# Kernel tuning notes

Hardware: AMD Instinct MI355X
Metric: run time of the kernel (lower is better)

The kernel has to match this reference:

```python
import jax, jax.numpy as jnp
import numpy as np


def setup_inputs() -> dict:
    key = jax.random.key(0)
    ks = jax.random.split(key, 6)
    B, T, D, H = 2, 2048, 1024, 16
    dk = D // H
    s = 0.02
    return {
        "x": jax.random.normal(ks[0], (B, T, D), dtype=jnp.float32),
        "Wq": jax.random.normal(ks[1], (H, dk, dk), dtype=jnp.float32) * s,
        "Wk": jax.random.normal(ks[2], (H, dk, dk), dtype=jnp.float32) * s,
        "Wv": jax.random.normal(ks[3], (H, dk, dk), dtype=jnp.float32) * s,
        "Wp": jax.random.normal(ks[4], (D, D), dtype=jnp.float32) * s,
        "bp": jnp.zeros((D,), dtype=jnp.float32),
    }


def reference(x, Wq, Wk, Wv, Wp, bp):
    B, T, D = x.shape
    H, dk, _ = Wq.shape
    # split into heads: [B, H, T, dk]
    xh = x.reshape(B, T, H, dk).transpose(0, 2, 1, 3)
    # per-head torch Linear (y = x @ W^T), all heads at once
    q = jnp.einsum('bhtd,hkd->bhtk', xh, Wq)
    k = jnp.einsum('bhtd,hkd->bhtk', xh, Wk)
    v = jnp.einsum('bhtd,hkd->bhtk', xh, Wv)
    scale = 1.0 / jnp.sqrt(jnp.float32(dk))  # original divides by sqrt(C) with C == d_k
    scores = jnp.einsum('bhqd,bhkd->bhqk', q, k) * scale
    causal = jnp.tril(jnp.ones((T, T), dtype=bool))
    scores = jnp.where(causal[None, None], scores, -jnp.inf)
    attn = jax.nn.softmax(scores, axis=-1)
    out = jnp.einsum('bhqk,bhkd->bhqd', attn, v)  # [B,H,T,dk]
    out = out.transpose(0, 2, 1, 3).reshape(B, T, D)  # concat heads
    return out @ Wp.T + bp
```

## Files before the change

kernel.cpp:

```cpp
#include <hip/hip_runtime.h>
#include <math.h>

#define B_ 2
#define T_ 2048
#define D_ 1024
#define H_ 16
#define DK 64
#define BH_ (B_*H_)

typedef __attribute__((ext_vector_type(8))) short short8;
typedef __attribute__((ext_vector_type(4))) float fragC;

#define MFMA32(A,B,C) __builtin_amdgcn_mfma_f32_16x16x32_bf16((A),(B),(C),0,0,0)

#if defined(__HIP_DEVICE_COMPILE__) && __has_builtin(__builtin_amdgcn_exp2f)
#define EXP2 __builtin_amdgcn_exp2f
#else
#define EXP2 exp2f
#endif

__device__ __forceinline__ unsigned short f2bf(float x) {
    union { float f; unsigned u; } c; c.f = x;
    unsigned r = c.u + 0x7fff + ((c.u >> 16) & 1);
    return (unsigned short)(r >> 16);
}

__device__ __forceinline__ unsigned pack2bf(float a, float b) {
    return (unsigned)f2bf(a) | ((unsigned)f2bf(b) << 16);
}

__device__ __forceinline__ unsigned permpack(float a, float b) {
    union { float f; unsigned u; } ca, cb; ca.f = a; cb.f = b;
    return __builtin_amdgcn_perm(cb.u, ca.u, 0x07060302);
}

__device__ __forceinline__ float truncbf(float x) {
    union { float f; unsigned u; } c; c.f = x;
    c.u &= 0xffff0000u;
    return c.f;
}

__device__ __forceinline__ short8 packbf8(float4 a, float4 b) {
    union { short8 v; unsigned u[4]; } r;
    r.u[0] = pack2bf(a.x, a.y); r.u[1] = pack2bf(a.z, a.w);
    r.u[2] = pack2bf(b.x, b.y); r.u[3] = pack2bf(b.z, b.w);
    return r.v;
}

__device__ __forceinline__ void gload_lds16(const void* g, void* l) {
    __builtin_amdgcn_global_load_lds(
        (const __attribute__((address_space(1))) unsigned int*)g,
        (__attribute__((address_space(3))) unsigned int*)l, 16, 0, 0);
}

__global__ __launch_bounds__(256) void qkv_kernel(
    const float* __restrict__ x,
    const float* __restrict__ Wq, const float* __restrict__ Wk,
    const float* __restrict__ Wv, const float* __restrict__ Wp,
    unsigned short* __restrict__ Wb,
    unsigned short* __restrict__ q, unsigned short* __restrict__ k,
    unsigned short* __restrict__ vt)
{
    __shared__ unsigned short Wl[3*64*64];

    const int bh = blockIdx.x;
    const int b  = bh >> 4, h = bh & 15;
    const int t0 = blockIdx.y * 128;
    const int tid = threadIdx.x;
    const int wave = tid >> 6, lane = tid & 63;
    const int n = lane & 15, quad = lane >> 4;

    {
        const int L = bh + (blockIdx.y << 5);
        const float* src = Wp + (size_t)L*2048 + tid*8;
        float4 a = *(const float4*)src;
        float4 b2 = *(const float4*)(src + 4);
        *(uint4*)(Wb + (size_t)L*2048 + tid*8) =
            make_uint4(pack2bf(a.x, a.y), pack2bf(a.z, a.w),
                       pack2bf(b2.x, b2.y), pack2bf(b2.z, b2.w));
    }

    #pragma unroll
    for (int mat = 0; mat < 3; ++mat) {
        const float* ws = ((mat == 0) ? Wq : (mat == 1) ? Wk : Wv)
                          + (size_t)h * 4096;
        #pragma unroll
        for (int j = 0; j < 2; ++j) {
            const int e = (j*256 + tid) * 8;
            float4 a = *(const float4*)&ws[e];
            float4 b2 = *(const float4*)&ws[e + 4];
            *(uint4*)&Wl[mat*4096 + e] =
                make_uint4(pack2bf(a.x, a.y), pack2bf(a.z, a.w),
                           pack2bf(b2.x, b2.y), pack2bf(b2.z, b2.w));
        }
    }

    const int tw = t0 + wave*32;
    short8 xf[2][2];
    #pragma unroll
    for (int rt = 0; rt < 2; ++rt) {
        const float* xr = &x[((size_t)b*T_ + tw + rt*16 + n)*D_ + h*DK];
        float4 a0 = *(const float4*)&xr[quad*8];
        float4 a1 = *(const float4*)&xr[quad*8 + 4];
        xf[rt][0] = packbf8(a0, a1);
        float4 b0 = *(const float4*)&xr[32 + quad*8];
        float4 b1 = *(const float4*)&xr[32 + quad*8 + 4];
        xf[rt][1] = packbf8(b0, b1);
    }
    __syncthreads();

    const float qsc = 0.125f * 1.44269504088896340736f;
    const int tb0 = blockIdx.y*8 + wave*2;
    #pragma unroll
    for (int mat = 0; mat < 3; ++mat) {
        const int wbase = mat * 4096;
        #pragma unroll
        for (int ct = 0; ct < 4; ++ct) {
            short8 wf0 = *(const short8*)&Wl[wbase + (ct*16 + n)*64 + quad*8];
            short8 wf1 = *(const short8*)&Wl[wbase + (ct*16 + n)*64 + 32 + quad*8];
            if (mat < 2) {
                #pragma unroll
                for (int rt = 0; rt < 2; ++rt) {
                    fragC z = {0.f,0.f,0.f,0.f};
                    z = MFMA32(wf0, xf[rt][0], z);
                    z = MFMA32(wf1, xf[rt][1], z);
                    if (mat == 0) {
                        z[0] *= qsc; z[1] *= qsc; z[2] *= qsc; z[3] *= qsc;
                    }
                    unsigned short* dstg = (mat == 0) ? q : k;
                    unsigned short* dp = &dstg[((size_t)bh*128 + tb0 + rt)*1024
                                               + (ct*2 + (quad>>1))*128 + n*8 + (quad&1)*4];
                    *(uint2*)dp = make_uint2(pack2bf(z[0], z[1]), pack2bf(z[2], z[3]));
                }
            } else {
                uint4 pv4;
                {
                    fragC z = {0.f,0.f,0.f,0.f};
                    z = MFMA32(xf[0][0], wf0, z);
                    z = MFMA32(xf[0][1], wf1, z);
                    pv4.x = pack2bf(z[0], z[1]); pv4.y = pack2bf(z[2], z[3]);
                }
                {
                    fragC z = {0.f,0.f,0.f,0.f};
                    z = MFMA32(xf[1][0], wf0, z);
                    z = MFMA32(xf[1][1], wf1, z);
                    pv4.z = pack2bf(z[0], z[1]); pv4.w = pack2bf(z[2], z[3]);
                }
                const int ktv = tw >> 6, pv = (tw >> 5) & 1;
                unsigned short* dp = &vt[(size_t)bh*131072 + ktv*4096
                                         + ct*1024 + pv*512 + lane*8];
                *(uint4*)dp = pv4;
            }
        }
    }
}

__global__ __launch_bounds__(256, 2) void attn_kernel(
    const unsigned short* __restrict__ q, const unsigned short* __restrict__ k,
    const unsigned short* __restrict__ vt, unsigned short* __restrict__ aout)
{
    __shared__ fragC Os[4][4][4][64];
    __shared__ float Ls[4][4][16];

    const int id = blockIdx.x;
    const int xc = id & 7, p = id >> 3;
    const int jj = p & 3, s = p >> 2, g = s & 7, r = s >> 3;
    const int bh = xc*4 + jj;
    const int qt = (r == 0) ? 31 - g : (r == 1) ? g : (r == 2) ? 23 - g : 8 + g;

    const int b   = bh >> 4, h = bh & 15;
    const int tid = threadIdx.x;
    const int w = tid >> 6, lane = tid & 63;
    const int n = lane & 15, quad = lane >> 4;

    short8 qf[4][2];
    #pragma unroll
    for (int qc = 0; qc < 4; ++qc) {
        const unsigned short* qb = &q[((size_t)bh*128 + qt*4 + qc)*1024 + n*8];
        qf[qc][0] = *(const short8*)&qb[quad*128];
        qf[qc][1] = *(const short8*)&qb[(4 + quad)*128];
    }

    fragC o[4][4];
    #pragma unroll
    for (int qc = 0; qc < 4; ++qc)
        #pragma unroll
        for (int dt = 0; dt < 4; ++dt) o[qc][dt] = (fragC){0.f,0.f,0.f,0.f};
    float lsc[4] = {0.f, 0.f, 0.f, 0.f};

    const unsigned short* kg = &k[(size_t)bh*131072 + lane*8];
    const unsigned short* vg = &vt[(size_t)bh*131072 + lane*8];
    const int nt = qt + 1;

    short8 kf[4][2];
    short8 vv[4][2];

    int t = w;
    if (t < nt) {
        #pragma unroll
        for (int ct = 0; ct < 4; ++ct) {
            kf[ct][0] = *(const short8*)&kg[t*4096 + ct*1024];
            kf[ct][1] = *(const short8*)&kg[t*4096 + ct*1024 + 512];
        }
        #pragma unroll
        for (int dt = 0; dt < 4; ++dt) {
            vv[dt][0] = *(const short8*)&vg[t*4096 + dt*1024];
            vv[dt][1] = *(const short8*)&vg[t*4096 + dt*1024 + 512];
        }
    }

    for (; t < nt; t += 4) {
        const bool diag = (t == qt);
        #pragma unroll
        for (int qc = 0; qc < 4; ++qc) {
            fragC c[4];
            __builtin_amdgcn_s_setprio(1);
            #pragma unroll
            for (int ct = 0; ct < 4; ++ct) {
                fragC z = {0.f,0.f,0.f,0.f};
                z = MFMA32(kf[ct][0], qf[qc][0], z);
                z = MFMA32(kf[ct][1], qf[qc][1], z);
                c[ct] = z;
            }
            __builtin_amdgcn_s_setprio(0);

            if (qc == 3 && t + 4 < nt) {
                #pragma unroll
                for (int ct = 0; ct < 4; ++ct) {
                    kf[ct][0] = *(const short8*)&kg[(t+4)*4096 + ct*1024];
                    kf[ct][1] = *(const short8*)&kg[(t+4)*4096 + ct*1024 + 512];
                }
            }

            union { unsigned u[4]; short8 v; } pb[2];
            float ls = 0.f;
            #pragma unroll
            for (int ct = 0; ct < 4; ++ct) {
                float p0 = EXP2(c[ct][0]), p1 = EXP2(c[ct][1]);
                float p2 = EXP2(c[ct][2]), p3 = EXP2(c[ct][3]);
                if (diag) {
                    const int lim = (qc*16 + n) - (ct*16 + quad*4);
                    if (0 > lim) p0 = 0.f;
                    if (1 > lim) p1 = 0.f;
                    if (2 > lim) p2 = 0.f;
                    if (3 > lim) p3 = 0.f;
                }
                p0 = truncbf(p0); p1 = truncbf(p1);
                p2 = truncbf(p2); p3 = truncbf(p3);
                ls += (p0 + p1) + (p2 + p3);
                pb[ct >> 1].u[(ct & 1)*2]     = permpack(p0, p1);
                pb[ct >> 1].u[(ct & 1)*2 + 1] = permpack(p2, p3);
            }
            lsc[qc] += ls;

            __builtin_amdgcn_s_setprio(1);
            #pragma unroll
            for (int pv = 0; pv < 2; ++pv) {
                #pragma unroll
                for (int dt = 0; dt < 4; ++dt)
                    o[qc][dt] = MFMA32(vv[dt][pv], pb[pv].v, o[qc][dt]);
            }
            __builtin_amdgcn_s_setprio(0);
        }

        if (t + 4 < nt) {
            #pragma unroll
            for (int dt = 0; dt < 4; ++dt) {
                vv[dt][0] = *(const short8*)&vg[(t+4)*4096 + dt*1024];
                vv[dt][1] = *(const short8*)&vg[(t+4)*4096 + dt*1024 + 512];
            }
        }
    }

    #pragma unroll
    for (int qc = 0; qc < 4; ++qc) {
        lsc[qc] += __shfl_xor(lsc[qc], 16);
        lsc[qc] += __shfl_xor(lsc[qc], 32);
    }

    #pragma unroll
    for (int qc = 0; qc < 4; ++qc) {
        #pragma unroll
        for (int dt = 0; dt < 4; ++dt)
            Os[w][qc][dt][lane] = o[qc][dt];
        if (quad == 0) Ls[w][qc][n] = lsc[qc];
    }
    __syncthreads();

    const float lsum = Ls[0][w][n] + Ls[1][w][n] + Ls[2][w][n] + Ls[3][w][n];
    const float inv = 1.0f / lsum;
    const int q0 = qt*64 + w*16;
    unsigned short* dp = &aout[((size_t)b*T_ + q0 + n)*D_ + h*DK + quad*4];
    #pragma unroll
    for (int dt = 0; dt < 4; ++dt) {
        fragC sum = Os[0][w][dt][lane] + Os[1][w][dt][lane]
                  + Os[2][w][dt][lane] + Os[3][w][dt][lane];
        *(uint2*)(dp + dt*16) =
            make_uint2(pack2bf(sum[0]*inv, sum[1]*inv),
                       pack2bf(sum[2]*inv, sum[3]*inv));
    }
}

__global__ __launch_bounds__(256, 3) void proj_kernel(
    const unsigned short* __restrict__ A, const unsigned short* __restrict__ Wb,
    const float* __restrict__ bp, float* __restrict__ out)
{
    __shared__ unsigned short As[2][64*64];
    __shared__ unsigned short Bs[2][128*64];

    const int id = blockIdx.x;
    const int xcd = id & 7, idx = id >> 3;
    const int m0 = (xcd*8 + (idx & 7)) * 64;
    const int n0 = (idx >> 3) * 128;
    const int tid = threadIdx.x;
    const int wave = tid >> 6, lane = tid & 63;
    const int wm = wave & 1, wn = wave >> 1;
    const int n = lane & 15, quad = lane >> 4;

    const int arow = tid >> 3, acol = (tid & 7) * 8;
    const unsigned short* ag = &A [(size_t)(m0 + arow)*1024 + acol];
    const unsigned short* bg = &Wb[(size_t)(n0 + arow)*1024 + acol];

    fragC acc[2][4];
    #pragma unroll
    for (int i = 0; i < 2; ++i)
        #pragma unroll
        for (int j = 0; j < 4; ++j) acc[i][j] = (fragC){0.f,0.f,0.f,0.f};

    auto stage = [&](int bu, int kt) {
        #pragma unroll
        for (int i2 = 0; i2 < 2; ++i2)
            gload_lds16(ag + (size_t)i2*32*1024 + kt*64, &As[bu][i2*2048 + tid*8]);
        #pragma unroll
        for (int j2 = 0; j2 < 4; ++j2)
            gload_lds16(bg + (size_t)j2*32*1024 + kt*64, &Bs[bu][j2*2048 + tid*8]);
    };

    stage(0, 0);
    for (int kt = 0; kt < 16; ++kt) {
        __syncthreads();
        if (kt < 15) stage((kt + 1) & 1, kt + 1);
        const unsigned short* Ab = As[kt & 1];
        const unsigned short* Bb = Bs[kt & 1];
        #pragma unroll
        for (int kk = 0; kk < 2; ++kk) {
            short8 af[2], bf[4];
            #pragma unroll
            for (int i = 0; i < 2; ++i)
                af[i] = *(const short8*)&Ab[(wm*32 + i*16 + n)*64 + kk*32 + quad*8];
            #pragma unroll
            for (int j = 0; j < 4; ++j)
                bf[j] = *(const short8*)&Bb[(wn*64 + j*16 + n)*64 + kk*32 + quad*8];
            #pragma unroll
            for (int i = 0; i < 2; ++i)
                #pragma unroll
                for (int j = 0; j < 4; ++j)
                    acc[i][j] = MFMA32(af[i], bf[j], acc[i][j]);
        }
    }

    #pragma unroll
    for (int i = 0; i < 2; ++i) {
        #pragma unroll
        for (int r = 0; r < 4; ++r) {
            const int m = m0 + wm*32 + i*16 + quad*4 + r;
            #pragma unroll
            for (int j = 0; j < 4; ++j) {
                const int col = n0 + wn*64 + j*16 + n;
                out[(size_t)m*1024 + col] = acc[i][j][r] + bp[col];
            }
        }
    }
}

extern "C" void kernel_launch(void* const* d_in, const int* in_sizes, int n_in,
                              void* d_out, int out_size, void* d_ws, size_t ws_size,
                              hipStream_t stream)
{
    const float* x  = (const float*)d_in[0];
    const float* Wq = (const float*)d_in[1];
    const float* Wk = (const float*)d_in[2];
    const float* Wv = (const float*)d_in[3];
    const float* Wp = (const float*)d_in[4];
    const float* bp = (const float*)d_in[5];
    float* out = (float*)d_out;

    const size_t per = (size_t)BH_ * T_ * DK;
    unsigned short* qws   = (unsigned short*)d_ws;
    unsigned short* kws   = qws + per;
    unsigned short* vtws  = kws + per;
    unsigned short* aws   = vtws + per;
    unsigned short* wbws  = aws + per;

    qkv_kernel<<<dim3(BH_, T_/128), 256, 0, stream>>>(x, Wq, Wk, Wv, Wp, wbws,
                                                      qws, kws, vtws);
    attn_kernel<<<dim3(1024), 256, 0, stream>>>(qws, kws, vtws, aws);
    proj_kernel<<<dim3(512), 256, 0, stream>>>(aws, wbws, bp, out);
}
```

Before: 130.8 us.

## Double-buffer K tiles and interleave QK MFMA with softmax in attention

```diff
diff --git a/kernel.cpp b/kernel.cpp
--- a/kernel.cpp
+++ b/kernel.cpp
@@ -155,6 +155,80 @@
     }
 }
 
+
+#define LOADK(KF, TT)                                                        \
+    _Pragma("unroll")                                                        \
+    for (int ct = 0; ct < 4; ++ct) {                                         \
+        KF[ct][0] = *(const short8*)&kg[(size_t)(TT)*4096 + ct*1024];        \
+        KF[ct][1] = *(const short8*)&kg[(size_t)(TT)*4096 + ct*1024 + 512];  \
+    }
+
+#define LOADV(TT)                                                            \
+    _Pragma("unroll")                                                        \
+    for (int dt = 0; dt < 4; ++dt) {                                         \
+        vv[dt][0] = *(const short8*)&vg[(size_t)(TT)*4096 + dt*1024];        \
+        vv[dt][1] = *(const short8*)&vg[(size_t)(TT)*4096 + dt*1024 + 512];  \
+    }
+
+#define SMAX(CV, CT, CP, SL)                                                 \
+    {                                                                        \
+        float p0 = EXP2(CV[0]), p1 = EXP2(CV[1]);                            \
+        float p2 = EXP2(CV[2]), p3 = EXP2(CV[3]);                            \
+        if (diag_) {                                                         \
+            const int lim = (qc*16 + n) - ((CT)*16 + quad*4);                \
+            if (0 > lim) p0 = 0.f;                                           \
+            if (1 > lim) p1 = 0.f;                                           \
+            if (2 > lim) p2 = 0.f;                                           \
+            if (3 > lim) p3 = 0.f;                                           \
+        }                                                                    \
+        p0 = truncbf(p0); p1 = truncbf(p1);                                  \
+        p2 = truncbf(p2); p3 = truncbf(p3);                                  \
+        ls += (p0 + p1) + (p2 + p3);                                         \
+        pb[CP].u[(SL)*2]     = permpack(p0, p1);                             \
+        pb[CP].u[(SL)*2 + 1] = permpack(p2, p3);                             \
+    }
+
+#define TILE_BODY(KF, PRE, TN, TT)                                           \
+  {                                                                          \
+    const bool diag_ = ((TT) == qt);                                         \
+    _Pragma("unroll")                                                        \
+    for (int qc = 0; qc < 4; ++qc) {                                         \
+        union { unsigned u[4]; short8 v; } pb[2];                            \
+        float ls = 0.f;                                                      \
+        _Pragma("unroll")                                                    \
+        for (int cp = 0; cp < 2; ++cp) {                                     \
+            fragC c0, c1;                                                    \
+            __builtin_amdgcn_s_setprio(1);                                   \
+            {                                                                \
+                fragC z = {0.f,0.f,0.f,0.f};                                 \
+                z = MFMA32(KF[cp*2][0], qf[qc][0], z);                       \
+                z = MFMA32(KF[cp*2][1], qf[qc][1], z);                       \
+                c0 = z;                                                      \
+            }                                                                \
+            {                                                                \
+                fragC z = {0.f,0.f,0.f,0.f};                                 \
+                z = MFMA32(KF[cp*2+1][0], qf[qc][0], z);                     \
+                z = MFMA32(KF[cp*2+1][1], qf[qc][1], z);                     \
+                c1 = z;                                                      \
+            }                                                                \
+            __builtin_amdgcn_s_setprio(0);                                   \
+            SMAX(c0, cp*2,     cp, 0)                                        \
+            SMAX(c1, cp*2 + 1, cp, 1)                                        \
+        }                                                                    \
+        lsc[qc] += ls;                                                       \
+        if (qc == 3 && (PRE)) { LOADK(KF, TN) }                              \
+        __builtin_amdgcn_s_setprio(1);                                       \
+        _Pragma("unroll")                                                    \
+        for (int pv = 0; pv < 2; ++pv) {                                     \
+            _Pragma("unroll")                                                \
+            for (int dt = 0; dt < 4; ++dt)                                   \
+                o[qc][dt] = MFMA32(vv[dt][pv], pb[pv].v, o[qc][dt]);         \
+        }                                                                    \
+        __builtin_amdgcn_s_setprio(0);                                       \
+    }                                                                        \
+    if ((TT) + 4 < nt) { LOADV((TT) + 4) }                                   \
+  }
+
 __global__ __launch_bounds__(256, 2) void attn_kernel(
     const unsigned short* __restrict__ q, const unsigned short* __restrict__ k,
     const unsigned short* __restrict__ vt, unsigned short* __restrict__ aout)
@@ -164,9 +238,9 @@
 
     const int id = blockIdx.x;
     const int xc = id & 7, p = id >> 3;
-    const int jj = p & 3, s = p >> 2, g = s & 7, r = s >> 3;
+    const int jj = p & 3, s = p >> 2, g = s & 7, r2 = s >> 3;
     const int bh = xc*4 + jj;
-    const int qt = (r == 0) ? 31 - g : (r == 1) ? g : (r == 2) ? 23 - g : 8 + g;
+    const int qt = (r2 == 0) ? 31 - g : (r2 == 1) ? g : (r2 == 2) ? 23 - g : 8 + g;
 
     const int b   = bh >> 4, h = bh & 15;
     const int tid = threadIdx.x;
@@ -192,85 +266,23 @@
     const unsigned short* vg = &vt[(size_t)bh*131072 + lane*8];
     const int nt = qt + 1;
 
-    short8 kf[4][2];
+    short8 kfA[4][2], kfB[4][2];
     short8 vv[4][2];
 
     int t = w;
-    if (t < nt) {
-        #pragma unroll
-        for (int ct = 0; ct < 4; ++ct) {
-            kf[ct][0] = *(const short8*)&kg[t*4096 + ct*1024];
-            kf[ct][1] = *(const short8*)&kg[t*4096 + ct*1024 + 512];
-        }
-        #pragma unroll
-        for (int dt = 0; dt < 4; ++dt) {
-            vv[dt][0] = *(const short8*)&vg[t*4096 + dt*1024];
-            vv[dt][1] = *(const short8*)&vg[t*4096 + dt*1024 + 512];
-        }
-    }
-
-    for (; t < nt; t += 4) {
-        const bool diag = (t == qt);
-        #pragma unroll
-        for (int qc = 0; qc < 4; ++qc) {
-            fragC c[4];
-            __builtin_amdgcn_s_setprio(1);
-            #pragma unroll
-            for (int ct = 0; ct < 4; ++ct) {
-                fragC z = {0.f,0.f,0.f,0.f};
-                z = MFMA32(kf[ct][0], qf[qc][0], z);
-                z = MFMA32(kf[ct][1], qf[qc][1], z);
-                c[ct] = z;
-            }
-            __builtin_amdgcn_s_setprio(0);
-
-            if (qc == 3 && t + 4 < nt) {
-                #pragma unroll
-                for (int ct = 0; ct < 4; ++ct) {
-                    kf[ct][0] = *(const short8*)&kg[(t+4)*4096 + ct*1024];
-                    kf[ct][1] = *(const short8*)&kg[(t+4)*4096 + ct*1024 + 512];
-                }
-            }
-
-            union { unsigned u[4]; short8 v; } pb[2];
-            float ls = 0.f;
-            #pragma unroll
-            for (int ct = 0; ct < 4; ++ct) {
-                float p0 = EXP2(c[ct][0]), p1 = EXP2(c[ct][1]);
-                float p2 = EXP2(c[ct][2]), p3 = EXP2(c[ct][3]);
-                if (diag) {
-                    const int lim = (qc*16 + n) - (ct*16 + quad*4);
-                    if (0 > lim) p0 = 0.f;
-                    if (1 > lim) p1 = 0.f;
-                    if (2 > lim) p2 = 0.f;
-                    if (3 > lim) p3 = 0.f;
-                }
-                p0 = truncbf(p0); p1 = truncbf(p1);
-                p2 = truncbf(p2); p3 = truncbf(p3);
-                ls += (p0 + p1) + (p2 + p3);
-                pb[ct >> 1].u[(ct & 1)*2]     = permpack(p0, p1);
-                pb[ct >> 1].u[(ct & 1)*2 + 1] = permpack(p2, p3);
-            }
-            lsc[qc] += ls;
-
-            __builtin_amdgcn_s_setprio(1);
-            #pragma unroll
-            for (int pv = 0; pv < 2; ++pv) {
-                #pragma unroll
-                for (int dt = 0; dt < 4; ++dt)
-                    o[qc][dt] = MFMA32(vv[dt][pv], pb[pv].v, o[qc][dt]);
-            }
-            __builtin_amdgcn_s_setprio(0);
-        }
-
-        if (t + 4 < nt) {
-            #pragma unroll
-            for (int dt = 0; dt < 4; ++dt) {
-                vv[dt][0] = *(const short8*)&vg[(t+4)*4096 + dt*1024];
-                vv[dt][1] = *(const short8*)&vg[(t+4)*4096 + dt*1024 + 512];
-            }
-        }
-    }
+    int ntw = (nt > w) ? ((nt - w + 3) >> 2) : 0;
+    if (ntw > 0) {
+        LOADV(t)
+        LOADK(kfA, t)
+        if (ntw > 1) { LOADK(kfB, t + 4) }
+    }
+    int i = 0;
+    while (i + 2 <= ntw) {
+        TILE_BODY(kfA, (i + 2 < ntw), t + 8,  t)
+        TILE_BODY(kfB, (i + 3 < ntw), t + 12, t + 4)
+        t += 8; i += 2;
+    }
+    if (i < ntw) { TILE_BODY(kfA, false, 0, t) }
 
     #pragma unroll
     for (int qc = 0; qc < 4; ++qc) {
```

Result: slower. 226.7 us (+73.3%).
